# Optimization experiments

Measured on AMD Instinct MI355X. Metric: run time of the kernel, lower is better.

## Reference

```python
import jax, jax.numpy as jnp
import numpy as np

B, S, HID = 1, 2048, 2048
NH, NKV = 16, 4
HD = HID // NH  # 128


def _rope_manual(x, cos_h, sin_h):
    # x: [B, S, nh, HD]; cos_h/sin_h: [1, S, 1, HD//2]
    d = x.shape[-1]
    x_rot = x[..., : d // 2]
    x_pass = x[..., d // 2:]
    # rotate interleaved pairs inside the first half
    x_rot = jnp.stack([-x_rot[..., 1::2], x_rot[..., ::2]], axis=-1)
    x_rot = x_rot.reshape(x_rot.shape[:-2] + (d // 2,))
    return jnp.concatenate(
        [x_rot * cos_h + x_pass * sin_h, -x_rot * sin_h + x_pass * cos_h], axis=-1
    )


def setup_inputs() -> dict:
    key = jax.random.key(0)
    ks = jax.random.split(key, 7)
    bound = 1.0 / np.sqrt(HID)
    return {
        "x": jax.random.normal(ks[0], (B, S, HID), jnp.float32),
        "cos": jax.random.uniform(ks[1], (S, HD), jnp.float32),
        "sin": jax.random.uniform(ks[2], (S, HD), jnp.float32),
        "wq": jax.random.uniform(ks[3], (NH * HD, HID), jnp.float32, -bound, bound),
        "wk": jax.random.uniform(ks[4], (NKV * HD, HID), jnp.float32, -bound, bound),
        "wv": jax.random.uniform(ks[5], (NKV * HD, HID), jnp.float32, -bound, bound),
        "wo": jax.random.uniform(ks[6], (HID, HID), jnp.float32, -bound, bound),
    }


def reference(x, cos, sin, wq, wk, wv, wo):
    b, s, _ = x.shape
    q = jnp.einsum("bsh,oh->bso", x, wq).reshape(b, s, NH, HD)
    k = jnp.einsum("bsh,oh->bso", x, wk).reshape(b, s, NKV, HD)
    v = jnp.einsum("bsh,oh->bso", x, wv).reshape(b, s, NKV, HD)

    cos_h = cos[None, :, None, : HD // 2]  # [1,S,1,HD/2]
    sin_h = sin[None, :, None, : HD // 2]
    q = _rope_manual(q, cos_h, sin_h)
    k = _rope_manual(k, cos_h, sin_h)

    # [B, H, S, D]
    q = q.transpose(0, 2, 1, 3)
    k = k.transpose(0, 2, 1, 3)
    v = v.transpose(0, 2, 1, 3)
    # GQA kv repeat (repeat_interleave over head dim)
    rep = NH // NKV
    k = jnp.repeat(k, rep, axis=1)
    v = jnp.repeat(v, rep, axis=1)

    scale = 1.0 / np.sqrt(HD).astype(np.float32)
    scores = jnp.einsum("bhqd,bhkd->bhqk", q, k) * scale
    causal = jnp.tril(jnp.ones((s, s), bool))
    scores = jnp.where(causal[None, None], scores, jnp.finfo(scores.dtype).min)
    attn = jax.nn.softmax(scores, axis=-1)
    out = jnp.einsum("bhqk,bhkd->bhqd", attn, v)  # [B,H,S,D]
    out = out.transpose(0, 2, 1, 3).reshape(b, s, NH * HD)
    return jnp.einsum("bso,ho->bsh", out, wo)
```

## Files before the change

kernel.cpp:

```cpp
#include <hip/hip_runtime.h>
#include <hip/hip_bf16.h>

typedef __bf16 bf16_t;
typedef __attribute__((ext_vector_type(8))) __bf16 bf16x8;
typedef __attribute__((ext_vector_type(4))) __bf16 bf16x4;
typedef __attribute__((ext_vector_type(4))) float f32x4;

#define S_LEN 2048
#define HID 2048
#define NH 16
#define NKV 4
#define HD 128

__device__ __forceinline__ void gll16(const bf16_t* g, bf16_t* l) {
    __builtin_amdgcn_global_load_lds(
        (const __attribute__((address_space(1))) unsigned int*)g,
        (__attribute__((address_space(3))) unsigned int*)l, 16, 0, 0);
}

__device__ __forceinline__ bf16x8 cvt2x4(float4 a, float4 b) {
    bf16x8 o;
    o[0]=(bf16_t)a.x; o[1]=(bf16_t)a.y; o[2]=(bf16_t)a.z; o[3]=(bf16_t)a.w;
    o[4]=(bf16_t)b.x; o[5]=(bf16_t)b.y; o[6]=(bf16_t)b.z; o[7]=(bf16_t)b.w;
    return o;
}

__global__ __launch_bounds__(256) void cvt_f32_bf16(const float* __restrict__ in,
                                                    bf16_t* __restrict__ out, int n)
{
    int i = (blockIdx.x * 256 + threadIdx.x) * 8;
    if (i >= n) return;
    float4 a = *(const float4*)&in[i];
    float4 b = *(const float4*)&in[i + 4];
    *(bf16x8*)&out[i] = cvt2x4(a, b);
}

__global__ __launch_bounds__(256) void cvt_w3(const float* __restrict__ wq,
                                              const float* __restrict__ wk,
                                              const float* __restrict__ wv,
                                              bf16_t* __restrict__ out)
{
    int i = (blockIdx.x * 256 + threadIdx.x) * 8;
    const float* src; int off;
    if (i < 4 * 1024 * 1024)      { src = wq; off = i; }
    else if (i < 5 * 1024 * 1024) { src = wk; off = i - 4 * 1024 * 1024; }
    else                          { src = wv; off = i - 5 * 1024 * 1024; }
    float4 a = *(const float4*)&src[off];
    float4 b = *(const float4*)&src[off + 4];
    *(bf16x8*)&out[i] = cvt2x4(a, b);
}

template<int MODE, typename CT>
__global__ __launch_bounds__(256, 4) void gemm128x64(
    const bf16_t* __restrict__ A, const bf16_t* __restrict__ B,
    CT* __restrict__ C, bf16_t* __restrict__ CkP, bf16_t* __restrict__ CvtP,
    int N, int K)
{
    __shared__ __align__(16) bf16_t sA[128 * 64];
    __shared__ __align__(16) bf16_t sB[64 * 64];

    const int tid = threadIdx.x, lane = tid & 63, wave = tid >> 6;
    const int l16 = lane & 15, quad = lane >> 4;
    const int m0 = blockIdx.y * 128, n0 = blockIdx.x * 64;
    const int wm = (wave >> 1) * 64, wn = (wave & 1) * 32;

    const bf16_t* gA[4]; const bf16_t* gB[2];
    bf16_t* lA[4]; bf16_t* lB[2];
#pragma unroll
    for (int t = 0; t < 4; t++) {
        int p = (wave * 4 + t) * 64 + lane;
        int row = p >> 3;
        int lc = (p & 7) ^ (row & 7);
        gA[t] = A + (size_t)(m0 + row) * K + lc * 8;
        lA[t] = &sA[(wave * 4 + t) * 512];
    }
#pragma unroll
    for (int t = 0; t < 2; t++) {
        int p = (wave * 2 + t) * 64 + lane;
        int row = p >> 3;
        int lc = (p & 7) ^ (row & 7);
        gB[t] = B + (size_t)(n0 + row) * K + lc * 8;
        lB[t] = &sB[(wave * 2 + t) * 512];
    }

    int offA[2][4], offB[2][2];
#pragma unroll
    for (int kc = 0; kc < 2; kc++) {
#pragma unroll
        for (int i = 0; i < 4; i++) {
            int rm = wm + i * 16 + l16;
            offA[kc][i] = rm * 64 + (((kc * 4 + quad) ^ (rm & 7)) * 8);
        }
#pragma unroll
        for (int j = 0; j < 2; j++) {
            int rn = wn + j * 16 + l16;
            offB[kc][j] = rn * 64 + (((kc * 4 + quad) ^ (rn & 7)) * 8);
        }
    }

    f32x4 acc[4][2] = {};

    for (int k0 = 0; k0 < K; k0 += 64) {
        __syncthreads();
#pragma unroll
        for (int t = 0; t < 4; t++) { gll16(gA[t], lA[t]); gA[t] += 64; }
#pragma unroll
        for (int t = 0; t < 2; t++) { gll16(gB[t], lB[t]); gB[t] += 64; }
        __syncthreads();

#pragma unroll
        for (int kc = 0; kc < 2; kc++) {
            bf16x8 af[4], bfv[2];
#pragma unroll
            for (int i = 0; i < 4; i++) af[i] = *(bf16x8*)&sA[offA[kc][i]];
#pragma unroll
            for (int j = 0; j < 2; j++) bfv[j] = *(bf16x8*)&sB[offB[kc][j]];
#pragma unroll
            for (int i = 0; i < 4; i++)
#pragma unroll
                for (int j = 0; j < 2; j++)
                    acc[i][j] = __builtin_amdgcn_mfma_f32_16x16x32_bf16(af[i], bfv[j], acc[i][j], 0, 0, 0);
        }
    }

#pragma unroll
    for (int i = 0; i < 4; i++) {
        int rowb = m0 + wm + i * 16 + quad * 4;
#pragma unroll
        for (int j = 0; j < 2; j++) {
            int col = n0 + wn + j * 16 + l16;
#pragma unroll
            for (int r = 0; r < 4; r++) {
                float v = acc[i][j][r];
                int row = rowb + r;
                if (MODE == 0) {
                    C[(size_t)row * N + col] = (CT)v;
                } else {
                    if (col < 2048)      C[(size_t)row * 2048 + col] = (CT)v;
                    else if (col < 2560) CkP[(size_t)row * 512 + (col - 2048)] = (bf16_t)v;
                    else                 CvtP[(size_t)(col - 2560) * S_LEN + row] = (bf16_t)v;
                }
            }
        }
    }
}

__global__ void rope_all(bf16_t* __restrict__ Qh, bf16_t* __restrict__ Kh,
                         const float* __restrict__ cosb, const float* __restrict__ sinb)
{
    int s = blockIdx.x;
    int grp = blockIdx.y;
    int sub = threadIdx.x >> 5;
    int i = threadIdx.x & 31;
    bf16_t* row = (grp < 4) ? (Qh + ((size_t)s * NH + grp * 4 + sub) * HD)
                            : (Kh + ((size_t)s * NKV + sub) * HD);
    float x0 = (float)row[2 * i];
    float x1 = (float)row[2 * i + 1];
    float p0 = (float)row[64 + 2 * i];
    float p1 = (float)row[64 + 2 * i + 1];
    float c0 = cosb[s * HD + 2 * i];
    float c1 = cosb[s * HD + 2 * i + 1];
    float n0 = sinb[s * HD + 2 * i];
    float n1 = sinb[s * HD + 2 * i + 1];
    float r0 = -x1, r1 = x0;
    row[2 * i]          = (bf16_t)(r0 * c0 + p0 * n0);
    row[2 * i + 1]      = (bf16_t)(r1 * c1 + p1 * n1);
    row[64 + 2 * i]     = (bf16_t)(-r0 * n0 + p0 * c0);
    row[64 + 2 * i + 1] = (bf16_t)(-r1 * n1 + p1 * c1);
}

__global__ __launch_bounds__(512, 1) void flash_attn8(
    const bf16_t* __restrict__ Q,
    const bf16_t* __restrict__ Kb,
    const bf16_t* __restrict__ VT,
    bf16_t* __restrict__ Opart,
    float* __restrict__ lpart,
    int S)
{
    __shared__ __align__(16) bf16_t sK[2][64 * 136];
    __shared__ __align__(16) bf16_t sVT[2][128 * 72];
    __shared__ __align__(16) bf16_t sP[8][16 * 72];

    const int qt  = blockIdx.x;
    const int kvh = blockIdx.y;
    const int z   = blockIdx.z;
    const int q0  = qt * 64;
    const int tid = threadIdx.x, lane = tid & 63, wave = tid >> 6;
    const int l16 = lane & 15, quad = lane >> 4;
    const int rowg = wave & 3;
    const int h0   = kvh * 4 + (wave >> 2) * 2;
    const float scale = 0.08838834764831845f;

    const int nkt = qt + 1;
    const int hc  = nkt >> 1;
    const int tb  = z ? hc : 0;
    const int te  = z ? nkt : hc;

    const int qrow = q0 + rowg * 16 + l16;

    bf16x8 qf[2][4];
#pragma unroll
    for (int h = 0; h < 2; h++)
#pragma unroll
        for (int c = 0; c < 4; c++)
            qf[h][c] = *(const bf16x8*)&Q[(size_t)qrow * HID + (h0 + h) * HD + c * 32 + quad * 8];

    f32x4 oacc[2][8] = {};
    float lsum[2] = {0.f, 0.f};

    int krow[2], kcol[2], vrow[2], vcol[2];
#pragma unroll
    for (int it = 0; it < 2; it++) {
        int c = tid + 512 * it;
        krow[it] = c >> 4; kcol[it] = (c & 15) * 8;
        vrow[it] = c >> 3; vcol[it] = (c & 7) * 8;
    }

    bf16x8 kpre[2], vpre[2];
#pragma unroll
    for (int it = 0; it < 2; it++) {
        kpre[it] = *(const bf16x8*)&Kb[(size_t)(tb * 64 + krow[it]) * (NKV * HD) + kvh * HD + kcol[it]];
        vpre[it] = *(const bf16x8*)&VT[((size_t)kvh * HD + vrow[it]) * S + tb * 64 + vcol[it]];
    }
#pragma unroll
    for (int it = 0; it < 2; it++) {
        *(bf16x8*)&sK[0][krow[it] * 136 + kcol[it]] = kpre[it];
        *(bf16x8*)&sVT[0][vrow[it] * 72 + vcol[it]] = vpre[it];
    }
    if (tb + 1 < te) {
        const int t1 = (tb + 1) * 64;
#pragma unroll
        for (int it = 0; it < 2; it++) {
            kpre[it] = *(const bf16x8*)&Kb[(size_t)(t1 + krow[it]) * (NKV * HD) + kvh * HD + kcol[it]];
            vpre[it] = *(const bf16x8*)&VT[((size_t)kvh * HD + vrow[it]) * S + t1 + vcol[it]];
        }
    }
    __syncthreads();

    int sel = 0;
    for (int kt = tb; kt < te; kt++) {
        const int t0 = kt * 64;
        const int ns = sel ^ 1;

        if (kt + 1 < te) {
#pragma unroll
            for (int it = 0; it < 2; it++) {
                *(bf16x8*)&sK[ns][krow[it] * 136 + kcol[it]] = kpre[it];
                *(bf16x8*)&sVT[ns][vrow[it] * 72 + vcol[it]] = vpre[it];
            }
            if (kt + 2 < te) {
                const int t2 = t0 + 128;
#pragma unroll
                for (int it = 0; it < 2; it++) {
                    kpre[it] = *(const bf16x8*)&Kb[(size_t)(t2 + krow[it]) * (NKV * HD) + kvh * HD + kcol[it]];
                    vpre[it] = *(const bf16x8*)&VT[((size_t)kvh * HD + vrow[it]) * S + t2 + vcol[it]];
                }
            }
        }

        f32x4 sc[2][4];
#pragma unroll
        for (int nt = 0; nt < 4; nt++) {
            bf16x8 kf[4];
#pragma unroll
            for (int c = 0; c < 4; c++)
                kf[c] = *(bf16x8*)&sK[sel][(nt * 16 + l16) * 136 + c * 32 + quad * 8];
#pragma unroll
            for (int h = 0; h < 2; h++) {
                f32x4 d = {};
#pragma unroll
                for (int c = 0; c < 4; c++)
                    d = __builtin_amdgcn_mfma_f32_16x16x32_bf16(kf[c], qf[h][c], d, 0, 0, 0);
                sc[h][nt] = d;
            }
        }

        bf16x8 pa[2][2];
        if (kt == qt) {
#pragma unroll
            for (int h = 0; h < 2; h++) {
#pragma unroll
                for (int nt = 0; nt < 4; nt++) {
                    const int tbk = t0 + nt * 16 + quad * 4;
                    bf16x4 pk;
#pragma unroll
                    for (int r = 0; r < 4; r++) {
                        float p = (tbk + r <= qrow) ? __expf(sc[h][nt][r] * scale) : 0.0f;
                        lsum[h] += p;
                        pk[r] = (bf16_t)p;
                    }
                    *(bf16x4*)&sP[wave][l16 * 72 + nt * 16 + quad * 4] = pk;
                }
#pragma unroll
                for (int kc = 0; kc < 2; kc++)
                    pa[h][kc] = *(bf16x8*)&sP[wave][l16 * 72 + kc * 32 + quad * 8];
            }
        } else {
#pragma unroll
            for (int h = 0; h < 2; h++) {
#pragma unroll
                for (int nt = 0; nt < 4; nt++) {
                    bf16x4 pk;
#pragma unroll
                    for (int r = 0; r < 4; r++) {
                        float p = __expf(sc[h][nt][r] * scale);
                        lsum[h] += p;
                        pk[r] = (bf16_t)p;
                    }
                    *(bf16x4*)&sP[wave][l16 * 72 + nt * 16 + quad * 4] = pk;
                }
#pragma unroll
                for (int kc = 0; kc < 2; kc++)
                    pa[h][kc] = *(bf16x8*)&sP[wave][l16 * 72 + kc * 32 + quad * 8];
            }
        }

#pragma unroll
        for (int dt = 0; dt < 8; dt++)
#pragma unroll
            for (int kc = 0; kc < 2; kc++) {
                bf16x8 vf = *(bf16x8*)&sVT[sel][(dt * 16 + l16) * 72 + kc * 32 + quad * 8];
#pragma unroll
                for (int h = 0; h < 2; h++)
                    oacc[h][dt] = __builtin_amdgcn_mfma_f32_16x16x32_bf16(pa[h][kc], vf, oacc[h][dt], 0, 0, 0);
            }

        __syncthreads();
        sel = ns;
    }

    bf16_t* Op = Opart + (size_t)z * S * HID;
#pragma unroll
    for (int h = 0; h < 2; h++) {
        float lr = lsum[h];
        lr += __shfl_xor(lr, 16, 64);
        lr += __shfl_xor(lr, 32, 64);
        if (quad == 0)
            lpart[((size_t)z * S + q0 + rowg * 16 + l16) * NH + (h0 + h)] = lr;
#pragma unroll
        for (int r = 0; r < 4; r++) {
            int srow = q0 + rowg * 16 + quad * 4 + r;
#pragma unroll
            for (int dt = 0; dt < 8; dt++)
                Op[(size_t)srow * HID + (h0 + h) * HD + dt * 16 + l16] =
                    (bf16_t)(oacc[h][dt][r]);
        }
    }
}

__global__ __launch_bounds__(256) void flash_combine(
    const bf16_t* __restrict__ Opart, const float* __restrict__ lpart,
    bf16_t* __restrict__ oh)
{
    int i = (blockIdx.x * 256 + threadIdx.x) * 8;
    int s = i >> 11;
    int h = (i >> 7) & 15;
    float l = lpart[(size_t)s * NH + h] + lpart[((size_t)S_LEN + s) * NH + h];
    float inv = 1.0f / l;
    bf16x8 a = *(const bf16x8*)&Opart[i];
    bf16x8 b = *(const bf16x8*)&Opart[(size_t)S_LEN * HID + i];
    bf16x8 o;
#pragma unroll
    for (int j = 0; j < 8; j++)
        o[j] = (bf16_t)(((float)a[j] + (float)b[j]) * inv);
    *(bf16x8*)&oh[i] = o;
}

extern "C" void kernel_launch(void* const* d_in, const int* in_sizes, int n_in,
                              void* d_out, int out_size, void* d_ws, size_t ws_size,
                              hipStream_t stream)
{
    const float* x    = (const float*)d_in[0];
    const float* cosb = (const float*)d_in[1];
    const float* sinb = (const float*)d_in[2];
    const float* wq   = (const float*)d_in[3];
    const float* wk   = (const float*)d_in[4];
    const float* wv   = (const float*)d_in[5];
    const float* wo   = (const float*)d_in[6];
    float* out = (float*)d_out;

    char* ws = (char*)d_ws;
    bf16_t* wb = (bf16_t*)(ws);
    bf16_t* qh = (bf16_t*)(ws + (size_t)12 * 1024 * 1024);
    bf16_t* kh = (bf16_t*)(ws + (size_t)20 * 1024 * 1024);
    bf16_t* vT = (bf16_t*)(ws + (size_t)22 * 1024 * 1024);
    float*  lp = (float*) (ws + (size_t)24 * 1024 * 1024);
    bf16_t* xb = (bf16_t*)d_out;
    bf16_t* op = (bf16_t*)d_out;

    const int NX = S_LEN * HID;

    cvt_f32_bf16<<<NX / (256 * 8), 256, 0, stream>>>(x, xb, NX);

    cvt_w3<<<6 * 1024 * 1024 / (256 * 8), 256, 0, stream>>>(wq, wk, wv, wb);

    gemm128x64<1, bf16_t><<<dim3(48, 16), 256, 0, stream>>>(xb, wb, qh, kh, vT, 3072, HID);

    rope_all<<<dim3(S_LEN, 5), 128, 0, stream>>>(qh, kh, cosb, sinb);

    flash_attn8<<<dim3(32, NKV, 2), 512, 0, stream>>>(qh, kh, vT, op, lp, S_LEN);

    flash_combine<<<NX / (256 * 8), 256, 0, stream>>>(op, lp, qh);

    cvt_f32_bf16<<<NX / (256 * 8), 256, 0, stream>>>(wo, wb, NX);

    gemm128x64<0, float><<<dim3(32, 16), 256, 0, stream>>>(qh, wb, out, nullptr, nullptr, HID, HID);
}
```

Before: 221.3 us.

## Balance causal attention work with variable KV splits per query tile

```diff
diff --git a/kernel.cpp b/kernel.cpp
--- a/kernel.cpp
+++ b/kernel.cpp
@@ -169,21 +169,29 @@
     row[64 + 2 * i + 1] = (bf16_t)(-r1 * n1 + p1 * c1);
 }
 
-__global__ __launch_bounds__(512, 1) void flash_attn8(
+__global__ __launch_bounds__(512, 4) void flash_attn9(
     const bf16_t* __restrict__ Q,
     const bf16_t* __restrict__ Kb,
     const bf16_t* __restrict__ VT,
-    bf16_t* __restrict__ Opart,
+    bf16_t* __restrict__ OpD,
+    bf16_t* __restrict__ OpX,
     float* __restrict__ lpart,
     int S)
 {
-    __shared__ __align__(16) bf16_t sK[2][64 * 136];
+    __shared__ __align__(16) bf16_t sK[64 * 136];
     __shared__ __align__(16) bf16_t sVT[2][128 * 72];
     __shared__ __align__(16) bf16_t sP[8][16 * 72];
 
-    const int qt  = blockIdx.x;
+    const int c   = blockIdx.x;
     const int kvh = blockIdx.y;
-    const int z   = blockIdx.z;
+    int qt = 0, cb = 0;
+    while (cb + 1 + (qt >> 3) <= c) { cb += 1 + (qt >> 3); qt++; }
+    const int ci     = c - cb;
+    const int splits = 1 + (qt >> 3);
+    const int ntiles = qt + 1;
+    const int tb = (ci * ntiles) / splits;
+    const int te = ((ci + 1) * ntiles) / splits;
+
     const int q0  = qt * 64;
     const int tid = threadIdx.x, lane = tid & 63, wave = tid >> 6;
     const int l16 = lane & 15, quad = lane >> 4;
@@ -191,19 +199,14 @@
     const int h0   = kvh * 4 + (wave >> 2) * 2;
     const float scale = 0.08838834764831845f;
 
-    const int nkt = qt + 1;
-    const int hc  = nkt >> 1;
-    const int tb  = z ? hc : 0;
-    const int te  = z ? nkt : hc;
-
     const int qrow = q0 + rowg * 16 + l16;
 
     bf16x8 qf[2][4];
 #pragma unroll
     for (int h = 0; h < 2; h++)
 #pragma unroll
-        for (int c = 0; c < 4; c++)
-            qf[h][c] = *(const bf16x8*)&Q[(size_t)qrow * HID + (h0 + h) * HD + c * 32 + quad * 8];
+        for (int cc = 0; cc < 4; cc++)
+            qf[h][cc] = *(const bf16x8*)&Q[(size_t)qrow * HID + (h0 + h) * HD + cc * 32 + quad * 8];
 
     f32x4 oacc[2][8] = {};
     float lsum[2] = {0.f, 0.f};
@@ -211,9 +214,9 @@
     int krow[2], kcol[2], vrow[2], vcol[2];
 #pragma unroll
     for (int it = 0; it < 2; it++) {
-        int c = tid + 512 * it;
-        krow[it] = c >> 4; kcol[it] = (c & 15) * 8;
-        vrow[it] = c >> 3; vcol[it] = (c & 7) * 8;
+        int cc = tid + 512 * it;
+        krow[it] = cc >> 4; kcol[it] = (cc & 15) * 8;
+        vrow[it] = cc >> 3; vcol[it] = (cc & 7) * 8;
     }
 
     bf16x8 kpre[2], vpre[2];
@@ -224,7 +227,7 @@
     }
 #pragma unroll
     for (int it = 0; it < 2; it++) {
-        *(bf16x8*)&sK[0][krow[it] * 136 + kcol[it]] = kpre[it];
+        *(bf16x8*)&sK[krow[it] * 136 + kcol[it]] = kpre[it];
         *(bf16x8*)&sVT[0][vrow[it] * 72 + vcol[it]] = vpre[it];
     }
     if (tb + 1 < te) {
@@ -242,10 +245,31 @@
         const int t0 = kt * 64;
         const int ns = sel ^ 1;
 
+        f32x4 sc[2][4];
+        __builtin_amdgcn_s_setprio(1);
+#pragma unroll
+        for (int nt = 0; nt < 4; nt++) {
+            bf16x8 kf[4];
+#pragma unroll
+            for (int cc = 0; cc < 4; cc++)
+                kf[cc] = *(bf16x8*)&sK[(nt * 16 + l16) * 136 + cc * 32 + quad * 8];
+#pragma unroll
+            for (int h = 0; h < 2; h++) {
+                f32x4 d = {};
+#pragma unroll
+                for (int cc = 0; cc < 4; cc++)
+                    d = __builtin_amdgcn_mfma_f32_16x16x32_bf16(kf[cc], qf[h][cc], d, 0, 0, 0);
+                sc[h][nt] = d;
+            }
+        }
+        __builtin_amdgcn_s_setprio(0);
+
+        __syncthreads();
+
         if (kt + 1 < te) {
 #pragma unroll
             for (int it = 0; it < 2; it++) {
-                *(bf16x8*)&sK[ns][krow[it] * 136 + kcol[it]] = kpre[it];
+                *(bf16x8*)&sK[krow[it] * 136 + kcol[it]] = kpre[it];
                 *(bf16x8*)&sVT[ns][vrow[it] * 72 + vcol[it]] = vpre[it];
             }
             if (kt + 2 < te) {
@@ -255,23 +279,6 @@
                     kpre[it] = *(const bf16x8*)&Kb[(size_t)(t2 + krow[it]) * (NKV * HD) + kvh * HD + kcol[it]];
                     vpre[it] = *(const bf16x8*)&VT[((size_t)kvh * HD + vrow[it]) * S + t2 + vcol[it]];
                 }
-            }
-        }
-
-        f32x4 sc[2][4];
-#pragma unroll
-        for (int nt = 0; nt < 4; nt++) {
-            bf16x8 kf[4];
-#pragma unroll
-            for (int c = 0; c < 4; c++)
-                kf[c] = *(bf16x8*)&sK[sel][(nt * 16 + l16) * 136 + c * 32 + quad * 8];
-#pragma unroll
-            for (int h = 0; h < 2; h++) {
-                f32x4 d = {};
-#pragma unroll
-                for (int c = 0; c < 4; c++)
-                    d = __builtin_amdgcn_mfma_f32_16x16x32_bf16(kf[c], qf[h][c], d, 0, 0, 0);
-                sc[h][nt] = d;
             }
         }
 
@@ -315,6 +322,7 @@
             }
         }
 
+        __builtin_amdgcn_s_setprio(1);
 #pragma unroll
         for (int dt = 0; dt < 8; dt++)
 #pragma unroll
@@ -324,45 +332,64 @@
                 for (int h = 0; h < 2; h++)
                     oacc[h][dt] = __builtin_amdgcn_mfma_f32_16x16x32_bf16(pa[h][kc], vf, oacc[h][dt], 0, 0, 0);
             }
+        __builtin_amdgcn_s_setprio(0);
 
         __syncthreads();
         sel = ns;
     }
 
-    bf16_t* Op = Opart + (size_t)z * S * HID;
+    const int sg = kvh * 80 + c;
+    bf16_t* Op = (sg < 256) ? (OpD + (size_t)sg * 32768)
+                            : (OpX + (size_t)(sg - 256) * 32768);
 #pragma unroll
     for (int h = 0; h < 2; h++) {
+        const int hl = (wave >> 2) * 2 + h;
         float lr = lsum[h];
         lr += __shfl_xor(lr, 16, 64);
         lr += __shfl_xor(lr, 32, 64);
         if (quad == 0)
-            lpart[((size_t)z * S + q0 + rowg * 16 + l16) * NH + (h0 + h)] = lr;
+            lpart[(size_t)sg * 256 + (rowg * 16 + l16) * 4 + hl] = lr;
 #pragma unroll
         for (int r = 0; r < 4; r++) {
-            int srow = q0 + rowg * 16 + quad * 4 + r;
+            int rr = rowg * 16 + quad * 4 + r;
 #pragma unroll
             for (int dt = 0; dt < 8; dt++)
-                Op[(size_t)srow * HID + (h0 + h) * HD + dt * 16 + l16] =
+                Op[((size_t)rr * 4 + hl) * 128 + dt * 16 + l16] =
                     (bf16_t)(oacc[h][dt][r]);
         }
     }
 }
 
-__global__ __launch_bounds__(256) void flash_combine(
-    const bf16_t* __restrict__ Opart, const float* __restrict__ lpart,
-    bf16_t* __restrict__ oh)
+__global__ __launch_bounds__(256) void flash_combine9(
+    const bf16_t* __restrict__ OpD, const bf16_t* __restrict__ OpX,
+    const float* __restrict__ lpart, bf16_t* __restrict__ oh)
 {
     int i = (blockIdx.x * 256 + threadIdx.x) * 8;
     int s = i >> 11;
     int h = (i >> 7) & 15;
-    float l = lpart[(size_t)s * NH + h] + lpart[((size_t)S_LEN + s) * NH + h];
+    int col = i & 127;
+    int qt = s >> 6;
+    int f = qt >> 3;
+    int base = qt + 4 * f * (f - 1) + (qt & 7) * f;
+    int splits = 1 + f;
+    int s0 = (h >> 2) * 80 + base;
+    int roff = (s & 63) * 4 + (h & 3);
+    float acc[8] = {0.f, 0.f, 0.f, 0.f, 0.f, 0.f, 0.f, 0.f};
+    float l = 0.f;
+    for (int ci = 0; ci < splits; ci++) {
+        int sg = s0 + ci;
+        const bf16_t* P = (sg < 256) ? (OpD + (size_t)sg * 32768)
+                                     : (OpX + (size_t)(sg - 256) * 32768);
+        bf16x8 a = *(const bf16x8*)&P[(size_t)roff * 128 + col];
+#pragma unroll
+        for (int j = 0; j < 8; j++) acc[j] += (float)a[j];
+        l += lpart[(size_t)sg * 256 + roff];
+    }
     float inv = 1.0f / l;
-    bf16x8 a = *(const bf16x8*)&Opart[i];
-    bf16x8 b = *(const bf16x8*)&Opart[(size_t)S_LEN * HID + i];
     bf16x8 o;
 #pragma unroll
     for (int j = 0; j < 8; j++)
-        o[j] = (bf16_t)(((float)a[j] + (float)b[j]) * inv);
+        o[j] = (bf16_t)(acc[j] * inv);
     *(bf16x8*)&oh[i] = o;
 }
 
@@ -385,8 +412,9 @@
     bf16_t* kh = (bf16_t*)(ws + (size_t)20 * 1024 * 1024);
     bf16_t* vT = (bf16_t*)(ws + (size_t)22 * 1024 * 1024);
     float*  lp = (float*) (ws + (size_t)24 * 1024 * 1024);
-    bf16_t* xb = (bf16_t*)d_out;
-    bf16_t* op = (bf16_t*)d_out;
+    bf16_t* opx = (bf16_t*)(ws + (size_t)24 * 1024 * 1024 + 512 * 1024);
+    bf16_t* xb  = (bf16_t*)d_out;
+    bf16_t* opd = (bf16_t*)d_out;
 
     const int NX = S_LEN * HID;
 
@@ -398,9 +426,9 @@
 
     rope_all<<<dim3(S_LEN, 5), 128, 0, stream>>>(qh, kh, cosb, sinb);
 
-    flash_attn8<<<dim3(32, NKV, 2), 512, 0, stream>>>(qh, kh, vT, op, lp, S_LEN);
-
-    flash_combine<<<NX / (256 * 8), 256, 0, stream>>>(op, lp, qh);
+    flash_attn9<<<dim3(80, NKV), 512, 0, stream>>>(qh, kh, vT, opd, opx, lp, S_LEN);
+
+    flash_combine9<<<NX / (256 * 8), 256, 0, stream>>>(opd, opx, lp, qh);
 
     cvt_f32_bf16<<<NX / (256 * 8), 256, 0, stream>>>(wo, wb, NX);
 
```

Result: slower. 345.4 us (+56.1%).
